# Kernel optimization log

Measured on AMD Instinct MI355X. Metric: run time of the kernel, lower is better.

The kernel has to match this reference:

```python
import jax, jax.numpy as jnp
import numpy as np

NEG_SLOPE = 0.2  # PyG GATConv default leaky_relu slope


def gat_conv(x, edge_index, W, a_src, a_dst, b):
    """PyG GATConv (heads=1, concat=True, add_self_loops=True, dropout=0)."""
    N = x.shape[0]
    loops = jnp.arange(N, dtype=edge_index.dtype)
    src = jnp.concatenate([edge_index[0], loops])  # [Ef]
    dst = jnp.concatenate([edge_index[1], loops])  # [Ef]
    h = x @ W  # [N, Dout]
    alpha_src = h @ a_src  # [N]
    alpha_dst = h @ a_dst  # [N]
    logits = jax.nn.leaky_relu(alpha_src[src] + alpha_dst[dst], NEG_SLOPE)  # [Ef]
    # segment softmax over edges grouped by destination node
    m = jax.ops.segment_max(logits, dst, num_segments=N)
    e = jnp.exp(logits - m[dst])
    denom = jax.ops.segment_sum(e, dst, num_segments=N)  # >0: every node has a self-loop
    alpha = e / denom[dst]  # [Ef]
    out = jax.ops.segment_sum(alpha[:, None] * h[src], dst, num_segments=N)
    return out + b


def global_mean_pool(x, batch, num_graphs):
    s = jax.ops.segment_sum(x, batch, num_segments=num_graphs)
    cnt = jax.ops.segment_sum(jnp.ones((x.shape[0],), x.dtype), batch, num_segments=num_graphs)
    return s / jnp.maximum(cnt, 1.0)[:, None]


NUM_GRAPHS = 64


def setup_inputs() -> dict:
    key = jax.random.key(0)
    ks = jax.random.split(key, 12)
    N, E, D = 50000, 600000, 128
    x = jax.random.normal(ks[0], (N, D), dtype=jnp.float32)
    edge_index = jax.random.randint(ks[1], (2, E), 0, N, dtype=jnp.int32)
    edge_weight = jax.random.uniform(ks[2], (E,), dtype=jnp.float32)
    batch = jnp.sort(jax.random.randint(ks[3], (N,), 0, NUM_GRAPHS, dtype=jnp.int32))
    sc = 1.0 / np.sqrt(D)
    W0 = jax.random.normal(ks[4], (D, D), dtype=jnp.float32) * sc
    a_src0 = jax.random.normal(ks[5], (D,), dtype=jnp.float32) * sc
    a_dst0 = jax.random.normal(ks[6], (D,), dtype=jnp.float32) * sc
    b0 = jnp.zeros((D,), dtype=jnp.float32)
    W1 = jax.random.normal(ks[7], (D, D), dtype=jnp.float32) * sc
    a_src1 = jax.random.normal(ks[8], (D,), dtype=jnp.float32) * sc
    a_dst1 = jax.random.normal(ks[9], (D,), dtype=jnp.float32) * sc
    b1 = jnp.zeros((D,), dtype=jnp.float32)
    return {"x": x, "edge_index": edge_index, "edge_weight": edge_weight, "batch": batch,
            "W0": W0, "a_src0": a_src0, "a_dst0": a_dst0, "b0": b0,
            "W1": W1, "a_src1": a_src1, "a_dst1": a_dst1, "b1": b1}


def reference(x, edge_index, edge_weight, batch, W0, a_src0, a_dst0, b0, W1, a_src1, a_dst1, b1):
    # layer 0 (relu_layers_index=[0] -> ReLU after layer 0)
    out = gat_conv(x, edge_index, W0, a_src0, a_dst0, b0)
    out = jax.nn.relu(out)
    emb0 = global_mean_pool(out, batch, NUM_GRAPHS)
    # layer 1 (no relu, no dropout)
    out = gat_conv(out, edge_index, W1, a_src1, a_dst1, b1)
    emb1 = global_mean_pool(out, batch, NUM_GRAPHS)
    return (emb0, emb1)
```

## Files before the change

kernel.cpp:

```cpp
#include <hip/hip_runtime.h>
#include <hip/hip_cooperative_groups.h>

typedef unsigned int u32;
typedef unsigned short u16;
typedef unsigned long long u64;

typedef short bf16x8 __attribute__((ext_vector_type(8)));
typedef float f32x4 __attribute__((ext_vector_type(4)));
typedef float f32x2 __attribute__((ext_vector_type(2)));

__device__ __forceinline__ float bl(u32 u){ return __uint_as_float(u << 16); }
__device__ __forceinline__ float bh(u32 u){ return __uint_as_float(u & 0xffff0000u); }
__device__ __forceinline__ float b16f(u16 r){ return __uint_as_float(((u32)r) << 16); }
__device__ __forceinline__ u16 f2b(float f){
  u32 u = __float_as_uint(f);
  u32 r = (u + 0x7fffu + ((u >> 16) & 1u)) >> 16;
  return (u16)r;
}
__device__ __forceinline__ u32 pk2(float a, float b){
  return (u32)f2b(a) | ((u32)f2b(b) << 16);
}
__device__ __forceinline__ void fma8(float* acc, float e2, uint2 h){
  f32x2 p0 = __builtin_amdgcn_cvt_pk_f32_fp8((int)h.x, 0);
  f32x2 p1 = __builtin_amdgcn_cvt_pk_f32_fp8((int)h.x, 1);
  f32x2 p2 = __builtin_amdgcn_cvt_pk_f32_fp8((int)h.y, 0);
  f32x2 p3 = __builtin_amdgcn_cvt_pk_f32_fp8((int)h.y, 1);
  acc[0]=fmaf(e2,p0.x,acc[0]); acc[1]=fmaf(e2,p0.y,acc[1]);
  acc[2]=fmaf(e2,p1.x,acc[2]); acc[3]=fmaf(e2,p1.y,acc[3]);
  acc[4]=fmaf(e2,p2.x,acc[4]); acc[5]=fmaf(e2,p2.y,acc[5]);
  acc[6]=fmaf(e2,p3.x,acc[6]); acc[7]=fmaf(e2,p3.y,acc[7]);
}

#define NEG_SLOPE 0.2f
#define BSTRIDE 4096
#define SMBYTES 34816



__device__ __forceinline__ int detect_body(const u32* __restrict__ x, char* SM){
  int* cnt_ = (int*)SM;
  if (threadIdx.x == 0) *cnt_ = 0;
  __syncthreads();
  u32 w = x[threadIdx.x];
  int e = (int)((w >> 7) & 0xFFu);
  if (e >= 110 && e <= 135) atomicAdd(cnt_, 1);
  __syncthreads();
  return (*cnt_ >= 128) ? 1 : 0;
}

__device__ __forceinline__ void bnd_body(const int* __restrict__ batch,
    int* __restrict__ bnd, int N)
{
  int g = threadIdx.x;
  if (g <= 64){
    int lo = 0, hi = N;
    while (lo < hi){ int mid = (lo + hi) >> 1; if (batch[mid] < g) lo = mid + 1; else hi = mid; }
    bnd[g] = lo;
  }
}

__device__ __forceinline__ void part_body(const int* __restrict__ ei, int E, int nbuck,
    int* __restrict__ gcnt, u64* __restrict__ breg, int job, char* SM)
{
  u64* stage = (u64*)SM;
  u32* hist  = (u32*)(SM + 16384);
  u32* lscan = (u32*)(SM + 17408);
  u32* gbase = (u32*)(SM + 18436);
  u32* cur   = (u32*)(SM + 19460);
  const int tid = threadIdx.x;
  __syncthreads();
  hist[tid] = 0; cur[tid] = 0;
  __syncthreads();
  const int e0 = job * 2048;
  int src[8], dst[8];
  #pragma unroll
  for (int j = 0; j < 8; j++){
    int t = e0 + tid + j*256;
    if (t < E){
      src[j] = ei[t]; dst[j] = ei[E + t];
      atomicAdd(&hist[dst[j] >> 8], 1u);
    } else dst[j] = -1;
  }
  __syncthreads();
  const u32 v = hist[tid];
  lscan[tid] = v;
  __syncthreads();
  for (int off = 1; off < 256; off <<= 1){
    u32 add = (tid >= off) ? lscan[tid - off] : 0;
    __syncthreads();
    lscan[tid] += add;
    __syncthreads();
  }
  if (tid == 255) lscan[256] = lscan[255];
  u32 excl = lscan[tid] - v;
  __syncthreads();
  const u32 total = lscan[256];
  lscan[tid] = excl;
  if (tid < nbuck && v > 0) gbase[tid] = (u32)atomicAdd(&gcnt[tid], (int)v);
  __syncthreads();
  #pragma unroll
  for (int j = 0; j < 8; j++){
    if (dst[j] >= 0){
      int b = dst[j] >> 8;
      u32 p = lscan[b] + atomicAdd(&cur[b], 1u);
      stage[p] = ((u64)(u32)dst[j] << 32) | (u32)src[j];
    }
  }
  __syncthreads();
  for (u32 i = tid; i < total; i += 256){
    u64 e = stage[i];
    int b = (int)(e >> 40);
    u32 r = i - lscan[b];
    breg[(long)b * BSTRIDE + gbase[b] + r] = e;
  }
}

__device__ __forceinline__ void csr_body(const int* __restrict__ gcnt,
    const u64* __restrict__ breg,
    int* __restrict__ rpd, int* __restrict__ csrc, int* __restrict__ csrc16,
    int N, int job, char* SM)
{
  u32* dl = (u32*)SM;
  u32* rp = dl + 256;
  u32* cu = rp + 256;
  const int b = job, tid = threadIdx.x;
  const int n0 = b << 8;
  __syncthreads();
  const int cntb = gcnt[b];
  dl[tid] = 0; cu[tid] = 0;
  __syncthreads();
  const u64* reg = breg + (long)b * BSTRIDE;
  for (int i = tid; i < cntb; i += 256)
    atomicAdd(&dl[(int)(reg[i] >> 32) - n0], 1u);
  __syncthreads();
  const u32 v = dl[tid];
  rp[tid] = v;
  __syncthreads();
  for (int off = 1; off < 256; off <<= 1){
    u32 add = (tid >= off) ? rp[tid - off] : 0;
    __syncthreads();
    rp[tid] += add;
    __syncthreads();
  }
  u32 excl = rp[tid] - v;
  __syncthreads();
  rp[tid] = excl;
  __syncthreads();
  int node = n0 + tid;
  if (node < N) rpd[node] = (int)(((u32)(b*BSTRIDE) + excl) | (v << 20));
  for (int i = tid; i < cntb; i += 256){
    u64 e = reg[i];
    int d = (int)(e >> 32) - n0;
    u32 li = atomicAdd(&cu[d], 1u);
    int s = (int)(e & 0xffffffffULL);
    if (li < 16) csrc16[((long)(n0 + d))*16 + li] = s;
    else         csrc[(long)b*BSTRIDE + rp[d] + li] = s;
  }
}

template<bool XEXT, bool KPERM>
__device__ __forceinline__ void gemm_body(int gb, int isbf,
    const void* __restrict__ Xv, const void* __restrict__ Wv,
    const void* __restrict__ av, const void* __restrict__ dv,
    u32* __restrict__ Hb, float* __restrict__ As, float* __restrict__ Ad, int N, char* SM)
{
  u16* Wt = (u16*)SM;
  const int tid = threadIdx.x;
  __syncthreads();

  if (isbf){
    const u32* Wp = (const u32*)Wv;
    #pragma unroll
    for (int i = 0; i < 16; i++){
      int idx = tid + i*256;
      u32 p = Wp[idx];
      int k = idx >> 6, n2 = idx & 63;
      int pos = KPERM ? ((k & 15)*8 + (k >> 4)) : k;
      Wt[(2*n2)*136 + pos]   = (u16)(p & 0xffffu);
      Wt[(2*n2+1)*136 + pos] = (u16)(p >> 16);
    }
  } else {
    const float* Wf = (const float*)Wv;
    #pragma unroll
    for (int i = 0; i < 64; i++){
      int idx = tid + i*256;
      int k = idx >> 7, n = idx & 127;
      int pos = KPERM ? ((k & 15)*8 + (k >> 4)) : k;
      Wt[n*136 + pos] = f2b(Wf[idx]);
    }
  }
  __syncthreads();

  const int wv = tid >> 6, L = tid & 63;
  const int row0 = (gb*4 + wv) * 16;
  if (row0 >= N) return;
  const int nl = L & 15, quad = L >> 4;

  bf16x8 af[4];
  if (!XEXT || isbf){
    const uint4* Xr = (const uint4*)(((const u32*)Xv) + (long)row0*64);
    #pragma unroll
    for (int kb = 0; kb < 4; kb++)
      af[kb] = *(const bf16x8*)&Xr[nl*16 + kb*4 + quad];
  } else {
    const float* Xf = ((const float*)Xv) + (long)(row0 + nl)*128;
    #pragma unroll
    for (int kb = 0; kb < 4; kb++){
      const float4* p = (const float4*)(Xf + kb*32 + quad*8);
      float4 f0 = p[0], f1 = p[1];
      uint4 tmp = make_uint4(pk2(f0.x,f0.y), pk2(f0.z,f0.w), pk2(f1.x,f1.y), pk2(f1.z,f1.w));
      af[kb] = *(const bf16x8*)&tmp;
    }
  }

  f32x4 acc[8];
  #pragma unroll
  for (int nt = 0; nt < 8; nt++) acc[nt] = (f32x4){0.f,0.f,0.f,0.f};
  #pragma unroll
  for (int nt = 0; nt < 8; nt++){
    #pragma unroll
    for (int kb = 0; kb < 4; kb++){
      bf16x8 bf = *(const bf16x8*)&Wt[(nt*16 + nl)*136 + kb*32 + quad*8];
      acc[nt] = __builtin_amdgcn_mfma_f32_16x16x32_bf16(af[kb], bf, acc[nt], 0, 0, 0);
    }
  }

  float ps[4] = {0.f,0.f,0.f,0.f}, pd[4] = {0.f,0.f,0.f,0.f};
  #pragma unroll
  for (int nt = 0; nt < 8; nt++){
    int col = nt*16 + nl;
    float a_ = isbf ? b16f(((const u16*)av)[col]) : ((const float*)av)[col];
    float d_ = isbf ? b16f(((const u16*)dv)[col]) : ((const float*)dv)[col];
    #pragma unroll
    for (int r = 0; r < 4; r++){
      ps[r] = fmaf(acc[nt][r], a_, ps[r]);
      pd[r] = fmaf(acc[nt][r], d_, pd[r]);
    }
  }
  #pragma unroll
  for (int off = 1; off < 16; off <<= 1){
    #pragma unroll
    for (int r = 0; r < 4; r++){
      ps[r] += __shfl_xor(ps[r], off);
      pd[r] += __shfl_xor(pd[r], off);
    }
  }
  if (nl == 0){
    #pragma unroll
    for (int r = 0; r < 4; r++){
      As[row0 + quad*4 + r] = ps[r];
      Ad[row0 + quad*4 + r] = pd[r];
    }
  }

  #pragma unroll
  for (int r = 0; r < 4; r++){
    long row = row0 + quad*4 + r;
    int w0 = 0, w1 = 0;
    w0 = __builtin_amdgcn_cvt_pk_fp8_f32(acc[0][r], acc[1][r], w0, 0);
    w0 = __builtin_amdgcn_cvt_pk_fp8_f32(acc[2][r], acc[3][r], w0, 1);
    w1 = __builtin_amdgcn_cvt_pk_fp8_f32(acc[4][r], acc[5][r], w1, 0);
    w1 = __builtin_amdgcn_cvt_pk_fp8_f32(acc[6][r], acc[7][r], w1, 1);
    uint2 v = make_uint2((u32)w0, (u32)w1);
    *(uint2*)(Hb + row*32 + nl*2) = v;
  }
}

__device__ __forceinline__ void pool_body(const u32* __restrict__ Ob,
    const int* __restrict__ bnd, float* __restrict__ psum, int N, int job, char* SM)
{
  int* bl_ = (int*)SM;
  const int tid = threadIdx.x;
  __syncthreads();
  if (tid < 65) bl_[tid] = bnd[tid];
  __syncthreads();
  const int wv = tid >> 6, lane = tid & 63;
  const int start = job * 128;
  const int end = min(start + 128, N);
  int node = start + wv;
  if (node >= end) return;
  int lo = 0, hi = 64;
  while (lo + 1 < hi){ int mid = (lo + hi) >> 1; if (bl_[mid] <= node) lo = mid; else hi = mid; }
  int cur = lo, nextb = bl_[cur + 1];
  float2 acc = make_float2(0.f, 0.f);
  const u32* __restrict__ ob = Ob + lane;
  for (int j = 0; j < 32; j += 4){
    int n0 = node + 4*j, n1 = n0 + 4, n2 = n0 + 8, n3 = n0 + 12;
    u32 p0 = 0, p1 = 0, p2 = 0, p3 = 0;
    if (n0 < end) p0 = ob[(long)n0*64];
    if (n1 < end) p1 = ob[(long)n1*64];
    if (n2 < end) p2 = ob[(long)n2*64];
    if (n3 < end) p3 = ob[(long)n3*64];
    #define PSTEP(nd, pv) \
      if (nd < end){ \
        while (nd >= nextb){ \
          atomicAdd(&psum[cur*128 + lane*2],     acc.x); \
          atomicAdd(&psum[cur*128 + lane*2 + 1], acc.y); \
          acc = make_float2(0.f, 0.f); \
          cur++; nextb = bl_[cur + 1]; \
        } \
        acc.x += bl(pv); acc.y += bh(pv); \
      }
    PSTEP(n0, p0) PSTEP(n1, p1) PSTEP(n2, p2) PSTEP(n3, p3)
    #undef PSTEP
  }
  atomicAdd(&psum[cur*128 + lane*2],     acc.x);
  atomicAdd(&psum[cur*128 + lane*2 + 1], acc.y);
}

template<bool RELU>
__device__ __forceinline__ void gath_body(const int* __restrict__ rpd,
    const int* __restrict__ csrc, const int* __restrict__ csrc16,
    const float* __restrict__ As, const float* __restrict__ Ad,
    const u32* __restrict__ Hb, const void* __restrict__ bv, int isbf,
    u32* __restrict__ Ob, int N, int job)
{
  long t = (long)job*256 + threadIdx.x;
  int node = (int)(t >> 4), q = (int)(t & 15);
  if (node >= N) return;
  const int base = threadIdx.x & 48;
  const u32 pk = (u32)rpd[node];
  const int c16 = csrc16[(long)node*16 + q];
  const float ad = Ad[node];
  const int dg = (int)(pk >> 20);
  const int* rowOv = csrc + (pk & 0xFFFFFu);
  float l = As[node] + ad;
  l = l > 0.f ? l : NEG_SLOPE * l;
  float e = __expf(l);
  float acc[8];
  {
    uint2 hv = ((const uint2*)(Hb + (long)node*32))[q];
    f32x2 p0 = __builtin_amdgcn_cvt_pk_f32_fp8((int)hv.x, 0);
    f32x2 p1 = __builtin_amdgcn_cvt_pk_f32_fp8((int)hv.x, 1);
    f32x2 p2 = __builtin_amdgcn_cvt_pk_f32_fp8((int)hv.y, 0);
    f32x2 p3 = __builtin_amdgcn_cvt_pk_f32_fp8((int)hv.y, 1);
    acc[0]=e*p0.x; acc[1]=e*p0.y; acc[2]=e*p1.x; acc[3]=e*p1.y;
    acc[4]=e*p2.x; acc[5]=e*p2.y; acc[6]=e*p3.x; acc[7]=e*p3.y;
  }
  float den = e;
  for (int jb = 0; jb < dg; jb += 16){
    int m = dg - jb; if (m > 16) m = 16;
    int sj = node;
    if (q < m) sj = (jb == 0) ? c16 : rowOv[jb + q];
    float asv = As[sj];
    int s[16];
    #pragma unroll
    for (int i = 0; i < 16; i++) s[i] = __shfl(sj, base + i);
    uint2 h[16];
    #pragma unroll
    for (int i = 0; i < 16; i++) h[i] = ((const uint2*)(Hb + (long)s[i]*32))[q];
    float evq = 0.f;
    if (q < m){
      float l2 = asv + ad;
      l2 = l2 > 0.f ? l2 : NEG_SLOPE * l2;
      evq = __expf(l2);
    }
    float ev[16];
    #pragma unroll
    for (int i = 0; i < 16; i++) ev[i] = __shfl(evq, base + i);
    float dsum = 0.f;
    #pragma unroll
    for (int i = 0; i < 16; i++) dsum += ev[i];
    den += dsum;
    #pragma unroll
    for (int i = 0; i < 16; i++) fma8(acc, ev[i], h[i]);
  }
  float inv = 1.f / den;
  float b[8];
  if (isbf){
    const u16* bp = (const u16*)bv;
    #pragma unroll
    for (int i = 0; i < 8; i++) b[i] = b16f(bp[i*16 + q]);
  } else {
    const float* bp = (const float*)bv;
    #pragma unroll
    for (int i = 0; i < 8; i++) b[i] = bp[i*16 + q];
  }
  float o[8];
  #pragma unroll
  for (int i = 0; i < 8; i++){
    o[i] = fmaf(acc[i], inv, b[i]);
    if (RELU) o[i] = fmaxf(o[i], 0.f);
  }
  uint4 w = make_uint4(pk2(o[0],o[1]), pk2(o[2],o[3]), pk2(o[4],o[5]), pk2(o[6],o[7]));
  *(uint4*)&Ob[(long)node*64 + q*4] = w;
}

__device__ __forceinline__ void fin_body(const float* __restrict__ ps0,
    const float* __restrict__ ps1, const int* __restrict__ bnd,
    int isbf, void* __restrict__ out, int job)
{
  int t = job*256 + threadIdx.x;
  if (t >= 8192) return;
  int g = t >> 7, pos = t & 127;
  int c = ((pos & 7) << 4) + (pos >> 3);
  int cc = bnd[g+1] - bnd[g];
  float cf = (float)(cc < 1 ? 1 : cc);
  float v0 = ps0[t] / cf, v1 = ps1[t] / cf;
  if (isbf){
    u16* o = (u16*)out;
    o[g*128 + c] = f2b(v0); o[8192 + g*128 + c] = f2b(v1);
  } else {
    float* o = (float*)out;
    o[g*128 + c] = v0; o[8192 + g*128 + c] = v1;
  }
}


struct MegaArgs {
  const u32* x; const int* ei; const int* batch;
  const void *W0, *as0, *ad0, *b0, *W1, *as1, *ad1, *b1;
  u32 *Hb, *Ob; float *As, *Ad;
  u64* breg; int *csrc, *csrc16, *rpd, *bnd, *gcnt;
  float *ps0, *ps1; void* out;
  int N, E, nbuck, gB, aB, nvB, pB;
};

__global__ __launch_bounds__(256) void mega_k(MegaArgs a)
{
  __shared__ __align__(16) char SM[SMBYTES];
  cooperative_groups::grid_group grid = cooperative_groups::this_grid();
  const int nb = (int)gridDim.x;
  const int isbf = detect_body(a.x, SM);

  for (int j = blockIdx.x; j < a.gB + 1 + a.aB; j += nb){
    if (j < a.gB)       gemm_body<true,false>(j, isbf, a.x, a.W0, a.as0, a.ad0, a.Hb, a.As, a.Ad, a.N, SM);
    else if (j == a.gB) bnd_body(a.batch, a.bnd, a.N);
    else                part_body(a.ei, a.E, a.nbuck, a.gcnt, a.breg, j - a.gB - 1, SM);
  }
  grid.sync();
  for (int j = blockIdx.x; j < a.nbuck; j += nb)
    csr_body(a.gcnt, a.breg, a.rpd, a.csrc, a.csrc16, a.N, j, SM);
  grid.sync();
  for (int j = blockIdx.x; j < a.nvB; j += nb)
    gath_body<true>(a.rpd, a.csrc, a.csrc16, a.As, a.Ad, a.Hb, a.b0, isbf, a.Ob, a.N, j);
  grid.sync();
  for (int j = blockIdx.x; j < a.pB + a.gB; j += nb){
    if (j < a.pB) pool_body(a.Ob, a.bnd, a.ps0, a.N, j, SM);
    else          gemm_body<false,true>(j - a.pB, isbf, a.Ob, a.W1, a.as1, a.ad1, a.Hb, a.As, a.Ad, a.N, SM);
  }
  grid.sync();
  for (int j = blockIdx.x; j < a.nvB; j += nb)
    gath_body<false>(a.rpd, a.csrc, a.csrc16, a.As, a.Ad, a.Hb, a.b1, isbf, a.Ob, a.N, j);
  grid.sync();
  for (int j = blockIdx.x; j < a.pB; j += nb)
    pool_body(a.Ob, a.bnd, a.ps1, a.N, j, SM);
  grid.sync();
  for (int j = blockIdx.x; j < 32; j += nb)
    fin_body(a.ps0, a.ps1, a.bnd, isbf, a.out, j);
}


__global__ __launch_bounds__(256) void gemmdet0_k(
    const u32* __restrict__ x, const int* __restrict__ batch, int* __restrict__ bnd,
    int* __restrict__ flag,
    const void* __restrict__ W0, const void* __restrict__ as0, const void* __restrict__ ad0,
    u32* __restrict__ Hb, float* __restrict__ As, float* __restrict__ Ad, int N, int gB)
{
  __shared__ __align__(16) char SM[SMBYTES];
  if ((int)blockIdx.x == gB){ bnd_body(batch, bnd, N); return; }
  int isbf = detect_body(x, SM);
  if (blockIdx.x == 0 && threadIdx.x == 0) *flag = isbf;
  gemm_body<true, false>(blockIdx.x, isbf, x, W0, as0, ad0, Hb, As, Ad, N, SM);
}

__global__ __launch_bounds__(256) void part_k(const int* __restrict__ ei, int E, int nbuck,
    int* __restrict__ gcnt, u64* __restrict__ breg)
{
  __shared__ __align__(16) char SM[SMBYTES];
  part_body(ei, E, nbuck, gcnt, breg, blockIdx.x, SM);
}

__global__ __launch_bounds__(256) void csr_k(const int* __restrict__ gcnt,
    const u64* __restrict__ breg,
    int* __restrict__ rpd, int* __restrict__ csrc, int* __restrict__ csrc16, int N)
{
  __shared__ __align__(16) char SM[SMBYTES];
  csr_body(gcnt, breg, rpd, csrc, csrc16, N, blockIdx.x, SM);
}

template<bool RELU>
__global__ __launch_bounds__(256) void gath_k(const int* __restrict__ rpd,
    const int* __restrict__ csrc, const int* __restrict__ csrc16,
    const float* __restrict__ As, const float* __restrict__ Ad,
    const u32* __restrict__ Hb, const void* __restrict__ bv, const int* __restrict__ flag,
    u32* __restrict__ Ob, int N)
{
  gath_body<RELU>(rpd, csrc, csrc16, As, Ad, Hb, bv, *flag, Ob, N, blockIdx.x);
}

__global__ __launch_bounds__(256) void poolgemm1_k(
    const u32* __restrict__ Ob, const int* __restrict__ bnd, float* __restrict__ ps0, int pB,
    const void* __restrict__ W1, const void* __restrict__ as1, const void* __restrict__ ad1,
    const int* __restrict__ flag,
    u32* __restrict__ Hb, float* __restrict__ As, float* __restrict__ Ad, int N)
{
  __shared__ __align__(16) char SM[SMBYTES];
  if ((int)blockIdx.x < pB){ pool_body(Ob, bnd, ps0, N, blockIdx.x, SM); return; }
  gemm_body<false, true>(blockIdx.x - pB, *flag, Ob, W1, as1, ad1, Hb, As, Ad, N, SM);
}

__global__ __launch_bounds__(256) void pool2_k(const u32* __restrict__ Ob,
    const int* __restrict__ bnd, float* __restrict__ psum, int N)
{
  __shared__ __align__(16) char SM[SMBYTES];
  pool_body(Ob, bnd, psum, N, blockIdx.x, SM);
}

__global__ __launch_bounds__(256) void fin_k(const float* __restrict__ ps0,
    const float* __restrict__ ps1, const int* __restrict__ bnd,
    const int* __restrict__ flag, void* __restrict__ out)
{
  fin_body(ps0, ps1, bnd, *flag, out, blockIdx.x);
}

extern "C" void kernel_launch(void* const* d_in, const int* in_sizes, int n_in,
                              void* d_out, int out_size, void* d_ws, size_t ws_size,
                              hipStream_t stream)
{
  const void* x    = d_in[0];
  const int* ei    = (const int*)d_in[1];
  const int* batch = (const int*)d_in[3];
  const void* W0  = d_in[4];
  const void* as0 = d_in[5];
  const void* ad0 = d_in[6];
  const void* b0  = d_in[7];
  const void* W1  = d_in[8];
  const void* as1 = d_in[9];
  const void* ad1 = d_in[10];
  const void* b1  = d_in[11];

  const int N  = in_sizes[0] / 128;
  const int E  = in_sizes[1] / 2;
  const int nbuck = (N + 255) >> 8;

  char* ws = (char*)d_ws;
  size_t off = 0;
  auto al = [&](size_t bytes){ size_t o = off; off += (bytes + 255) & ~(size_t)255; return o; };
  u32*   Hb    = (u32*)(ws + al((size_t)N*32*4));
  u32*   Ob    = (u32*)(ws + al((size_t)N*64*4));
  float* As    = (float*)(ws + al((size_t)N*4));
  float* Ad    = (float*)(ws + al((size_t)N*4));
  u64*   breg  = (u64*)(ws + al((size_t)nbuck*BSTRIDE*8));
  int*   csrc  = (int*)(ws + al((size_t)nbuck*BSTRIDE*4));
  int*   csrc16= (int*)(ws + al((size_t)N*16*4));
  int*   rpd   = (int*)(ws + al((size_t)N*4));
  int*   bnd   = (int*)(ws + al(512));
  const size_t zbytes = 2*64*128*4 + 256*4;
  char*  z0    = ws + al(zbytes);
  float* ps0   = (float*)z0;
  float* ps1   = ps0 + 8192;
  int*   gcnt  = (int*)(ps1 + 8192);
  int*   flag  = (int*)(ws + al(256));
  if (off > ws_size) return;

  hipMemsetAsync(z0, 0, zbytes, stream);

  const int gB   = (N/16 + 3) / 4;
  const int aB   = (E + 2047) / 2048;
  const int nvB16= (N*16 + 255) / 256;
  const int pB   = (N + 127) / 128;

  MegaArgs A;
  A.x = (const u32*)x; A.ei = ei; A.batch = batch;
  A.W0 = W0; A.as0 = as0; A.ad0 = ad0; A.b0 = b0;
  A.W1 = W1; A.as1 = as1; A.ad1 = ad1; A.b1 = b1;
  A.Hb = Hb; A.Ob = Ob; A.As = As; A.Ad = Ad;
  A.breg = breg; A.csrc = csrc; A.csrc16 = csrc16; A.rpd = rpd; A.bnd = bnd; A.gcnt = gcnt;
  A.ps0 = ps0; A.ps1 = ps1; A.out = d_out;
  A.N = N; A.E = E; A.nbuck = nbuck; A.gB = gB; A.aB = aB; A.nvB = nvB16; A.pB = pB;

  int occ = 0;
  hipError_t qerr = hipOccupancyMaxActiveBlocksPerMultiprocessor(
      &occ, (const void*)mega_k, 256, 0);
  if (qerr == hipSuccess && occ >= 1){
    int grid = occ * 256;
    if (grid > 512) grid = 512;
    void* kargs[] = { (void*)&A };
    hipError_t err = hipLaunchCooperativeKernel((const void*)mega_k,
        dim3(grid), dim3(256), kargs, 0, stream);
    if (err == hipSuccess) return;
  }

  gemmdet0_k<<<gB + 1, 256, 0, stream>>>((const u32*)x, batch, bnd, flag,
      W0, as0, ad0, Hb, As, Ad, N, gB);
  part_k<<<aB, 256, 0, stream>>>(ei, E, nbuck, gcnt, breg);
  csr_k<<<nbuck, 256, 0, stream>>>(gcnt, breg, rpd, csrc, csrc16, N);
  gath_k<true><<<nvB16, 256, 0, stream>>>(rpd, csrc, csrc16, As, Ad, Hb, b0, flag, Ob, N);
  poolgemm1_k<<<pB + gB, 256, 0, stream>>>(Ob, bnd, ps0, pB,
      W1, as1, ad1, flag, Hb, As, Ad, N);
  gath_k<false><<<nvB16, 256, 0, stream>>>(rpd, csrc, csrc16, As, Ad, Hb, b1, flag, Ob, N);
  pool2_k<<<pB, 256, 0, stream>>>(Ob, bnd, ps1, N);
  fin_k<<<32, 256, 0, stream>>>(ps0, ps1, bnd, flag, d_out);
}
```

Before: 182.3 us.

## Fuse global mean-pool into GAT gather epilogue and drop layer-1 output store

Mean pooling now happens inside the gather phase. Each block reduces its 16 nodes' outputs into shared memory with atomics, then adds the result to the per-graph sums in global memory, falling back to direct global atomics when the block spans more than two graphs. This removes the separate pool passes that re-read the node outputs. It also removes one grid-wide sync, and layer 1 no longer writes its node outputs at all. In exchange the gather phase picks up extra barriers and shared-memory atomics, and it relies on the batch vector being sorted so most blocks touch only one or two graphs.

After: 183.9 us. Within noise of the previous version (+0.9%).

```diff
diff --git a/kernel.cpp b/kernel.cpp
--- a/kernel.cpp
+++ b/kernel.cpp
@@ -308,82 +308,122 @@
   atomicAdd(&psum[cur*128 + lane*2 + 1], acc.y);
 }
 
-template<bool RELU>
+template<bool RELU, bool POOL, bool STOREOB>
 __device__ __forceinline__ void gath_body(const int* __restrict__ rpd,
     const int* __restrict__ csrc, const int* __restrict__ csrc16,
     const float* __restrict__ As, const float* __restrict__ Ad,
     const u32* __restrict__ Hb, const void* __restrict__ bv, int isbf,
-    u32* __restrict__ Ob, int N, int job)
+    u32* __restrict__ Ob, const int* __restrict__ batch, float* __restrict__ psum,
+    int N, int job, char* SM)
 {
   long t = (long)job*256 + threadIdx.x;
   int node = (int)(t >> 4), q = (int)(t & 15);
-  if (node >= N) return;
-  const int base = threadIdx.x & 48;
-  const u32 pk = (u32)rpd[node];
-  const int c16 = csrc16[(long)node*16 + q];
-  const float ad = Ad[node];
-  const int dg = (int)(pk >> 20);
-  const int* rowOv = csrc + (pk & 0xFFFFFu);
-  float l = As[node] + ad;
-  l = l > 0.f ? l : NEG_SLOPE * l;
-  float e = __expf(l);
-  float acc[8];
-  {
-    uint2 hv = ((const uint2*)(Hb + (long)node*32))[q];
-    f32x2 p0 = __builtin_amdgcn_cvt_pk_f32_fp8((int)hv.x, 0);
-    f32x2 p1 = __builtin_amdgcn_cvt_pk_f32_fp8((int)hv.x, 1);
-    f32x2 p2 = __builtin_amdgcn_cvt_pk_f32_fp8((int)hv.y, 0);
-    f32x2 p3 = __builtin_amdgcn_cvt_pk_f32_fp8((int)hv.y, 1);
-    acc[0]=e*p0.x; acc[1]=e*p0.y; acc[2]=e*p1.x; acc[3]=e*p1.y;
-    acc[4]=e*p2.x; acc[5]=e*p2.y; acc[6]=e*p3.x; acc[7]=e*p3.y;
-  }
-  float den = e;
-  for (int jb = 0; jb < dg; jb += 16){
-    int m = dg - jb; if (m > 16) m = 16;
-    int sj = node;
-    if (q < m) sj = (jb == 0) ? c16 : rowOv[jb + q];
-    float asv = As[sj];
-    int s[16];
-    #pragma unroll
-    for (int i = 0; i < 16; i++) s[i] = __shfl(sj, base + i);
-    uint2 h[16];
-    #pragma unroll
-    for (int i = 0; i < 16; i++) h[i] = ((const uint2*)(Hb + (long)s[i]*32))[q];
-    float evq = 0.f;
-    if (q < m){
-      float l2 = asv + ad;
-      l2 = l2 > 0.f ? l2 : NEG_SLOPE * l2;
-      evq = __expf(l2);
-    }
-    float ev[16];
-    #pragma unroll
-    for (int i = 0; i < 16; i++) ev[i] = __shfl(evq, base + i);
-    float dsum = 0.f;
-    #pragma unroll
-    for (int i = 0; i < 16; i++) dsum += ev[i];
-    den += dsum;
-    #pragma unroll
-    for (int i = 0; i < 16; i++) fma8(acc, ev[i], h[i]);
-  }
-  float inv = 1.f / den;
-  float b[8];
-  if (isbf){
-    const u16* bp = (const u16*)bv;
-    #pragma unroll
-    for (int i = 0; i < 8; i++) b[i] = b16f(bp[i*16 + q]);
-  } else {
-    const float* bp = (const float*)bv;
-    #pragma unroll
-    for (int i = 0; i < 8; i++) b[i] = bp[i*16 + q];
-  }
+  const bool act = node < N;
   float o[8];
-  #pragma unroll
-  for (int i = 0; i < 8; i++){
-    o[i] = fmaf(acc[i], inv, b[i]);
-    if (RELU) o[i] = fmaxf(o[i], 0.f);
-  }
-  uint4 w = make_uint4(pk2(o[0],o[1]), pk2(o[2],o[3]), pk2(o[4],o[5]), pk2(o[6],o[7]));
-  *(uint4*)&Ob[(long)node*64 + q*4] = w;
+  int gid = 0;
+  if (act){
+    const int base = threadIdx.x & 48;
+    const u32 pk = (u32)rpd[node];
+    const int c16 = csrc16[(long)node*16 + q];
+    if (POOL) gid = batch[node];
+    const float ad = Ad[node];
+    const int dg = (int)(pk >> 20);
+    const int* rowOv = csrc + (pk & 0xFFFFFu);
+    float l = As[node] + ad;
+    l = l > 0.f ? l : NEG_SLOPE * l;
+    float e = __expf(l);
+    float acc[8];
+    {
+      uint2 hv = ((const uint2*)(Hb + (long)node*32))[q];
+      f32x2 p0 = __builtin_amdgcn_cvt_pk_f32_fp8((int)hv.x, 0);
+      f32x2 p1 = __builtin_amdgcn_cvt_pk_f32_fp8((int)hv.x, 1);
+      f32x2 p2 = __builtin_amdgcn_cvt_pk_f32_fp8((int)hv.y, 0);
+      f32x2 p3 = __builtin_amdgcn_cvt_pk_f32_fp8((int)hv.y, 1);
+      acc[0]=e*p0.x; acc[1]=e*p0.y; acc[2]=e*p1.x; acc[3]=e*p1.y;
+      acc[4]=e*p2.x; acc[5]=e*p2.y; acc[6]=e*p3.x; acc[7]=e*p3.y;
+    }
+    float den = e;
+    const int dgc = dg;
+    for (int jb = 0; jb < dgc; jb += 16){
+      int m = dgc - jb; if (m > 16) m = 16;
+      int sj = node;
+      if (q < m) sj = (jb == 0) ? c16 : rowOv[jb + q];
+      float asv = As[sj];
+      int s[16];
+      #pragma unroll
+      for (int i = 0; i < 16; i++) s[i] = __shfl(sj, base + i);
+      uint2 h[16];
+      #pragma unroll
+      for (int i = 0; i < 16; i++) h[i] = ((const uint2*)(Hb + (long)s[i]*32))[q];
+      float evq = 0.f;
+      if (q < m){
+        float l2 = asv + ad;
+        l2 = l2 > 0.f ? l2 : NEG_SLOPE * l2;
+        evq = __expf(l2);
+      }
+      float ev[16];
+      #pragma unroll
+      for (int i = 0; i < 16; i++) ev[i] = __shfl(evq, base + i);
+      float dsum = 0.f;
+      #pragma unroll
+      for (int i = 0; i < 16; i++) dsum += ev[i];
+      den += dsum;
+      #pragma unroll
+      for (int i = 0; i < 16; i++) fma8(acc, ev[i], h[i]);
+    }
+    float inv = 1.f / den;
+    float b[8];
+    if (isbf){
+      const u16* bp = (const u16*)bv;
+      #pragma unroll
+      for (int i = 0; i < 8; i++) b[i] = b16f(bp[i*16 + q]);
+    } else {
+      const float* bp = (const float*)bv;
+      #pragma unroll
+      for (int i = 0; i < 8; i++) b[i] = bp[i*16 + q];
+    }
+    #pragma unroll
+    for (int i = 0; i < 8; i++){
+      o[i] = fmaf(acc[i], inv, b[i]);
+      if (RELU) o[i] = fmaxf(o[i], 0.f);
+    }
+    if (STOREOB){
+      uint4 w = make_uint4(pk2(o[0],o[1]), pk2(o[2],o[3]), pk2(o[4],o[5]), pk2(o[6],o[7]));
+      *(uint4*)&Ob[(long)node*64 + q*4] = w;
+    }
+  }
+
+  if constexpr (POOL){
+    float* sred = (float*)SM;
+    int*   sg   = (int*)(SM + 1024);
+    const int tid = threadIdx.x;
+    const int nb16 = job * 16;
+    __syncthreads();
+    if (tid == 0){
+      sg[0] = batch[nb16 < N ? nb16 : N-1];
+      int nlast = nb16 + 15; if (nlast >= N) nlast = N - 1;
+      sg[1] = batch[nlast];
+    }
+    sred[tid] = 0.f;
+    __syncthreads();
+    const int gmin = sg[0], gmax = sg[1];
+    if (gmax - gmin <= 1){
+      if (act){
+        int sel = gid - gmin;
+        #pragma unroll
+        for (int i = 0; i < 8; i++)
+          atomicAdd(&sred[sel*128 + q*8 + i], o[i]);
+      }
+      __syncthreads();
+      int sel2 = tid >> 7, c = tid & 127;
+      if (sel2 <= gmax - gmin)
+        atomicAdd(&psum[(gmin + sel2)*128 + c], sred[tid]);
+    } else if (act){
+      #pragma unroll
+      for (int i = 0; i < 8; i++)
+        atomicAdd(&psum[gid*128 + q*8 + i], o[i]);
+    }
+  }
 }
 
 __device__ __forceinline__ void fin_body(const float* __restrict__ ps0,
@@ -433,18 +473,15 @@
     csr_body(a.gcnt, a.breg, a.rpd, a.csrc, a.csrc16, a.N, j, SM);
   grid.sync();
   for (int j = blockIdx.x; j < a.nvB; j += nb)
-    gath_body<true>(a.rpd, a.csrc, a.csrc16, a.As, a.Ad, a.Hb, a.b0, isbf, a.Ob, a.N, j);
+    gath_body<true,true,true>(a.rpd, a.csrc, a.csrc16, a.As, a.Ad, a.Hb, a.b0,
+        isbf, a.Ob, a.batch, a.ps0, a.N, j, SM);
   grid.sync();
-  for (int j = blockIdx.x; j < a.pB + a.gB; j += nb){
-    if (j < a.pB) pool_body(a.Ob, a.bnd, a.ps0, a.N, j, SM);
-    else          gemm_body<false,true>(j - a.pB, isbf, a.Ob, a.W1, a.as1, a.ad1, a.Hb, a.As, a.Ad, a.N, SM);
-  }
+  for (int j = blockIdx.x; j < a.gB; j += nb)
+    gemm_body<false,true>(j, isbf, a.Ob, a.W1, a.as1, a.ad1, a.Hb, a.As, a.Ad, a.N, SM);
   grid.sync();
   for (int j = blockIdx.x; j < a.nvB; j += nb)
-    gath_body<false>(a.rpd, a.csrc, a.csrc16, a.As, a.Ad, a.Hb, a.b1, isbf, a.Ob, a.N, j);
-  grid.sync();
-  for (int j = blockIdx.x; j < a.pB; j += nb)
-    pool_body(a.Ob, a.bnd, a.ps1, a.N, j, SM);
+    gath_body<false,true,false>(a.rpd, a.csrc, a.csrc16, a.As, a.Ad, a.Hb, a.b1,
+        isbf, a.Ob, a.batch, a.ps1, a.N, j, SM);
   grid.sync();
   for (int j = blockIdx.x; j < 32; j += nb)
     fin_body(a.ps0, a.ps1, a.bnd, isbf, a.out, j);
@@ -486,7 +523,8 @@
     const u32* __restrict__ Hb, const void* __restrict__ bv, const int* __restrict__ flag,
     u32* __restrict__ Ob, int N)
 {
-  gath_body<RELU>(rpd, csrc, csrc16, As, Ad, Hb, bv, *flag, Ob, N, blockIdx.x);
+  gath_body<RELU, false, true>(rpd, csrc, csrc16, As, Ad, Hb, bv, *flag, Ob,
+      (const int*)nullptr, (float*)nullptr, N, blockIdx.x, (char*)nullptr);
 }
 
 __global__ __launch_bounds__(256) void poolgemm1_k(
```
